# Kernel optimization log

Hardware: AMD Instinct MI355X
Metric: run time of the kernel (lower is better)

Reference implementation:

```python
import jax, jax.numpy as jnp
import numpy as np
import math

KERNEL_SIZES = [3, 5, 7, 7, 9, 9]
DILATIONS = [1, 2, 1, 3, 1, 2]
NUM_HEADS = 6
HEAD_DIM = 32  # in_channels 192 / 6 heads


def _neighborhood_patches(t, k, dil):
    """Equivalent of F.unfold(t, kernel_size=k, dilation=dil, padding=dil*(k//2)).
    t: [B, d, H, W] -> [B, d, k*k, H, W] (zero-padded borders, torch unfold ordering:
    patch index p = i*k + j over the kernel window, row-major)."""
    B, d, H, W = t.shape
    pad = dil * (k // 2)
    tp = jnp.pad(t, ((0, 0), (0, 0), (pad, pad), (pad, pad)))
    pats = [tp[:, :, i * dil:i * dil + H, j * dil:j * dil + W]
            for i in range(k) for j in range(k)]
    return jnp.stack(pats, axis=2)


def setup_inputs() -> dict:
    key = jax.random.key(0)
    ks = jax.random.split(key, 3 + NUM_HEADS)
    B, C, H, W = 4, 192, 96, 96
    x = jax.random.normal(ks[0], (B, C, H, W), dtype=jnp.float32)
    w_qkv = jax.random.normal(ks[1], (3 * C, C), dtype=jnp.float32) * 0.02  # 1x1 conv weight
    w_out = jax.random.normal(ks[2], (C, C), dtype=jnp.float32) * 0.02      # 1x1 conv weight
    inp = {"x": x, "w_qkv": w_qkv, "w_out": w_out}
    for i, k in enumerate(KERNEL_SIZES):
        # module inits biases to zeros; use small randn so softmax path is exercised
        inp[f"b{i}"] = jax.random.normal(ks[3 + i], (k * k,), dtype=jnp.float32) * 0.02
    return inp


def reference(x, w_qkv, w_out, b0, b1, b2, b3, b4, b5):
    biases = [b0, b1, b2, b3, b4, b5]
    B, C, H, W = x.shape
    scale = 1.0 / math.sqrt(HEAD_DIM)
    # 1x1 conv qkv projection
    qkv = jnp.einsum('bchw,oc->bohw', x, w_qkv)
    q, k, v = jnp.split(qkv, 3, axis=1)
    q = q.reshape(B, NUM_HEADS, HEAD_DIM, H, W)
    k = k.reshape(B, NUM_HEADS, HEAD_DIM, H, W)
    v = v.reshape(B, NUM_HEADS, HEAD_DIM, H, W)
    head_outs = []
    for i in range(NUM_HEADS):  # heads have structurally different (k, dilation)
        ksz, dil = KERNEL_SIZES[i], DILATIONS[i]
        kp = _neighborhood_patches(k[:, i], ksz, dil)  # [B, d, k*k, H, W]
        vp = _neighborhood_patches(v[:, i], ksz, dil)  # [B, d, k*k, H, W]
        scores = jnp.einsum('bdhw,bdphw->bphw', q[:, i], kp) * scale
        scores = scores + biases[i][None, :, None, None]
        attn = jax.nn.softmax(scores, axis=1)  # softmax over the k*k neighborhood
        head_outs.append(jnp.einsum('bphw,bdphw->bdhw', attn, vp))
    out = jnp.concatenate(head_outs, axis=1)  # [B, C, H, W]
    return jnp.einsum('bchw,oc->bohw', out, w_out)
```

## Files before the change

### kernel.cpp

```cpp
#include <hip/hip_runtime.h>
#include <hip/hip_bf16.h>
#include <math.h>

#define NPIX 9216
#define HDIM 96
#define WDIM 96
#define NHEADS 6
#define BATCH 4

typedef _Float16 f16x8 __attribute__((ext_vector_type(8)));
typedef float    f32x4 __attribute__((ext_vector_type(4)));

struct Bias6 { const float* p[6]; };

__device__ __forceinline__ void cp16(void* ldst, const void* gsrc) {
    __builtin_amdgcn_global_load_lds(
        (const __attribute__((address_space(1))) unsigned int*)gsrc,
        (__attribute__((address_space(3))) unsigned int*)ldst, 16, 0, 0);
}

__device__ __forceinline__ unsigned packf16(float a, float b) {
    _Float16 ha = (_Float16)a, hb = (_Float16)b;
    return (unsigned)*(unsigned short*)&ha | ((unsigned)*(unsigned short*)&hb << 16);
}

template<int N>
__device__ __forceinline__ void waitcnt_vm() {
    if constexpr (N == 0) asm volatile("s_waitcnt vmcnt(0)" ::: "memory");
    else if constexpr (N == 2) asm volatile("s_waitcnt vmcnt(2)" ::: "memory");
    else if constexpr (N == 3) asm volatile("s_waitcnt vmcnt(3)" ::: "memory");
    else if constexpr (N == 5) asm volatile("s_waitcnt vmcnt(5)" ::: "memory");
    else asm volatile("s_waitcnt vmcnt(0)" ::: "memory");
    __builtin_amdgcn_sched_barrier(0);
}

#define MIX_LL(acc, kk, qq) asm("v_fma_mix_f32 %0, %1, %2, %0 op_sel:[0,0,0] op_sel_hi:[1,1,0]" : "+v"(acc) : "v"(kk), "v"(qq))
#define MIX_HH(acc, kk, qq) asm("v_fma_mix_f32 %0, %1, %2, %0 op_sel:[1,1,0] op_sel_hi:[1,1,0]" : "+v"(acc) : "v"(kk), "v"(qq))
#define MIX_LF(acc, vv, ee) asm("v_fma_mix_f32 %0, %1, %2, %0 op_sel:[0,0,0] op_sel_hi:[1,0,0]" : "+v"(acc) : "v"(vv), "v"(ee))
#define MIX_HF(acc, vv, ee) asm("v_fma_mix_f32 %0, %1, %2, %0 op_sel:[1,0,0] op_sel_hi:[1,0,0]" : "+v"(acc) : "v"(vv), "v"(ee))

__global__ __launch_bounds__(256) void convert_x(
    const float* __restrict__ x, _Float16* __restrict__ Xf,
    const float* __restrict__ w1, _Float16* __restrict__ Wf1,
    const float* __restrict__ w2, _Float16* __restrict__ Wf2,
    uint4* __restrict__ guard)
{
    __shared__ float t[32][65];
    const int b  = blockIdx.z;
    const int c0 = blockIdx.y * 32;
    const int p0 = blockIdx.x * 64;
    const int tid = threadIdx.x;

    if (blockIdx.y == 0 && blockIdx.z == 0) {
        const int f = blockIdx.x * 256 + tid;
        #pragma unroll
        for (int u = 0; u < 4; ++u) {
            const int i = f * 4 + u;
            if (i < 576 * 192) Wf1[i] = (_Float16)w1[i];
            else               Wf2[i - 576 * 192] = (_Float16)w2[i - 576 * 192];
        }
        if (blockIdx.x == 0 && tid < 64)
            guard[tid] = make_uint4(0u, 0u, 0u, 0u);
    }

    const int pl = tid & 63;
    #pragma unroll
    for (int i = 0; i < 8; ++i) {
        const int c = i * 4 + (tid >> 6);
        t[c][pl] = x[((size_t)b * 192 + c0 + c) * NPIX + p0 + pl];
    }
    __syncthreads();
    const int p  = tid >> 2;
    const int cq = (tid & 3) * 8;
    f16x8 vh;
    #pragma unroll
    for (int j = 0; j < 8; ++j)
        vh[j] = (_Float16)t[cq + j][p];
    *(f16x8*)(Xf + ((size_t)b * NPIX + p0 + p) * 192 + c0 + cq) = vh;
}

template<int MODE, int M>
__global__ __launch_bounds__(256) void gemm_mfma(
    const _Float16* __restrict__ A, const _Float16* __restrict__ B,
    void* __restrict__ Yv)
{
    constexpr int MT = M / 64;
    __shared__ _Float16 sA[64 * 64];
    __shared__ _Float16 sB[128 * 64];

    const int orig = blockIdx.x;
    const int xcd = orig & 7;
    const int l = orig >> 3;
    const int m0 = (l % MT) * 64;
    const int b  = (l / MT) & 3;
    const int n0 = (xcd * 9 + l / (MT * 4)) * 128;

    const int tid  = threadIdx.x;
    const int lane = tid & 63;
    const int wid  = tid >> 6;
    const int wr = wid >> 1, wc = wid & 1;
    const int lr = lane & 15;
    const int kg = lane >> 4;

    const char* gA = (const char*)A + (size_t)m0 * 384;
    const char* gB = (const char*)B + ((size_t)b * NPIX + n0) * 384;

    f32x4 acc[2][4];
    #pragma unroll
    for (int mf = 0; mf < 2; ++mf)
        #pragma unroll
        for (int nf = 0; nf < 4; ++nf)
            acc[mf][nf] = (f32x4){0.f, 0.f, 0.f, 0.f};

    for (int ks = 0; ks < 3; ++ks) {
        if (ks) __syncthreads();
        const int kb = ks * 128;
        #pragma unroll
        for (int it = 0; it < 2; ++it) {
            const int d  = it * 256 + tid;
            const int rd = d >> 3, cd = d & 7;
            const size_t src = (size_t)rd * 384 + kb + ((cd ^ (rd & 7)) << 4);
            cp16((char*)sA + d * 16, gA + src);
        }
        #pragma unroll
        for (int it = 0; it < 4; ++it) {
            const int d  = it * 256 + tid;
            const int rd = d >> 3, cd = d & 7;
            const size_t src = (size_t)rd * 384 + kb + ((cd ^ (rd & 7)) << 4);
            cp16((char*)sB + d * 16, gB + src);
        }
        __syncthreads();
        #pragma unroll
        for (int s = 0; s < 2; ++s) {
            f16x8 aH[2], bH[4];
            #pragma unroll
            for (int mf = 0; mf < 2; ++mf) {
                const int row = wr * 32 + mf * 16 + lr;
                const int c = (s * 4 + kg) ^ (row & 7);
                aH[mf] = *(const f16x8*)((const char*)sA + row * 128 + c * 16);
            }
            #pragma unroll
            for (int nf = 0; nf < 4; ++nf) {
                const int row = wc * 64 + nf * 16 + lr;
                const int c = (s * 4 + kg) ^ (row & 7);
                bH[nf] = *(const f16x8*)((const char*)sB + row * 128 + c * 16);
            }
            #pragma unroll
            for (int mf = 0; mf < 2; ++mf)
                #pragma unroll
                for (int nf = 0; nf < 4; ++nf)
                    acc[mf][nf] = __builtin_amdgcn_mfma_f32_16x16x32_f16(aH[mf], bH[nf], acc[mf][nf], 0, 0, 0);
        }
    }

    if (MODE == 0) {
        float* Yb = (float*)Yv + ((size_t)b * M + m0 + wr * 32) * NPIX + n0 + wc * 64;
        #pragma unroll
        for (int mf = 0; mf < 2; ++mf)
            #pragma unroll
            for (int r = 0; r < 4; ++r) {
                const int row = mf * 16 + kg * 4 + r;
                #pragma unroll
                for (int nf = 0; nf < 4; ++nf)
                    Yb[(size_t)row * NPIX + nf * 16 + lr] = acc[mf][nf][r];
            }
    } else {
        #pragma unroll
        for (int mf = 0; mf < 2; ++mf) {
            const int cbase = m0 + wr * 32 + mf * 16 + kg * 4;
            unsigned* Yq = (unsigned*)Yv
                + (((size_t)b * 72 + (cbase >> 3)) * NPIX + n0 + wc * 64 + lr) * 4
                + ((kg & 1) << 1);
            #pragma unroll
            for (int nf = 0; nf < 4; ++nf) {
                Yq[(nf * 16) * 4 + 0] = packf16(acc[mf][nf][0], acc[mf][nf][1]);
                Yq[(nf * 16) * 4 + 1] = packf16(acc[mf][nf][2], acc[mf][nf][3]);
            }
        }
    }
}

template<int KSZ, int DIL, bool DB, int L>
__device__ __forceinline__ void attn_body(
    const uint4* __restrict__ Qq, const uint4* __restrict__ Kq,
    const uint4* __restrict__ Vq, const float* __restrict__ bias,
    const uint4* __restrict__ guard,
    _Float16* __restrict__ oh, int h0, int w0,
    uint4* __restrict__ bufs,
    unsigned (* __restrict__ out_lds)[256])
{
    constexpr int CC  = KSZ / 2;
    constexpr int HAL = CC * DIL;
    constexpr int R   = 8 + 2 * HAL;
    constexpr int C   = 32 + 2 * HAL;
    constexpr int RC  = R * C;
    constexpr int NN  = KSZ * KSZ;

    const int tid = threadIdx.x;
    const int tx = tid & 31;
    const int ty = tid >> 5;
    const int pix = (h0 + ty) * WDIM + (w0 + tx);
    const int lb = ty * C + tx;

    uint4 qv[4];
    #pragma unroll
    for (int p = 0; p < 4; ++p) qv[p] = Qq[(size_t)p * NPIX + pix];

    float score[NN];
    #pragma unroll
    for (int n = 0; n < NN; ++n) score[n] = bias[n] * 5.656854249492381f;

    auto STAGE = [&](int r) {
        const uint4* src = (r < 4) ? (Kq + (size_t)r * NPIX)
                                   : (Vq + (size_t)(r - 4) * NPIX);
        uint4* dst = bufs + (DB ? ((r & 1) * (L * 256)) : 0);
        #pragma unroll
        for (int it = 0; it < L; ++it) {
            const int idx = it * 256 + tid;
            const int rr = idx / C, cc = idx - rr * C;
            const int gh = h0 - HAL + rr, gw = w0 - HAL + cc;
            const bool ok = (idx < RC) && ((unsigned)gh < (unsigned)HDIM)
                                       && ((unsigned)gw < (unsigned)WDIM);
            const uint4* s = ok ? (src + gh * WDIM + gw) : guard;
            cp16(dst + idx, s);
        }
    };

    auto QK = [&](const uint4* buf, int oct) {
        const uint4 q = qv[oct];
        #pragma unroll
        for (int i = 0; i < KSZ; ++i)
            #pragma unroll
            for (int j = 0; j < KSZ; ++j) {
                const uint4 k8 = buf[lb + i * DIL * C + j * DIL];
                float s = score[i * KSZ + j];
                MIX_LL(s, k8.x, q.x); MIX_HH(s, k8.x, q.x);
                MIX_LL(s, k8.y, q.y); MIX_HH(s, k8.y, q.y);
                MIX_LL(s, k8.z, q.z); MIX_HH(s, k8.z, q.z);
                MIX_LL(s, k8.w, q.w); MIX_HH(s, k8.w, q.w);
                score[i * KSZ + j] = s;
            }
    };

    float inv = 0.f;
    auto SOFTMAX = [&]() {
        float l = 0.f;
        #pragma unroll
        for (int n = 0; n < NN; ++n) {
            const float e = exp2f(score[n] * 0.25506113952980654f);
            l += e;
            score[n] = e;
        }
        inv = 1.f / l;
    };

    auto PV = [&](const uint4* buf, int oct) {
        float a0 = 0.f, a1 = 0.f, a2 = 0.f, a3 = 0.f;
        float a4 = 0.f, a5 = 0.f, a6 = 0.f, a7 = 0.f;
        #pragma unroll
        for (int i = 0; i < KSZ; ++i)
            #pragma unroll
            for (int j = 0; j < KSZ; ++j) {
                const uint4 v8 = buf[lb + i * DIL * C + j * DIL];
                const float e = score[i * KSZ + j];
                MIX_LF(a0, v8.x, e); MIX_HF(a1, v8.x, e);
                MIX_LF(a2, v8.y, e); MIX_HF(a3, v8.y, e);
                MIX_LF(a4, v8.z, e); MIX_HF(a5, v8.z, e);
                MIX_LF(a6, v8.w, e); MIX_HF(a7, v8.w, e);
            }
        const int rr = oct & 1;
        out_lds[rr * 4 + 0][tid] = packf16(a0 * inv, a1 * inv);
        out_lds[rr * 4 + 1][tid] = packf16(a2 * inv, a3 * inv);
        out_lds[rr * 4 + 2][tid] = packf16(a4 * inv, a5 * inv);
        out_lds[rr * 4 + 3][tid] = packf16(a6 * inv, a7 * inv);
    };

    auto COOP = [&](int half) {
        #pragma unroll
        for (int it = 0; it < 2; ++it) {
            const int linear = it * 256 + tid;
            const int px = linear >> 1;
            const int c  = linear & 1;
            const int gpix = (h0 + (px >> 5)) * WDIM + w0 + (px & 31);
            uint4 val = make_uint4(out_lds[c * 4 + 0][px], out_lds[c * 4 + 1][px],
                                   out_lds[c * 4 + 2][px], out_lds[c * 4 + 3][px]);
            *((uint4*)((unsigned*)(oh + (size_t)gpix * 192)) + half * 2 + c) = val;
        }
    };

    if constexpr (DB) {
        STAGE(0);
        #pragma unroll
        for (int r = 0; r < 8; ++r) {
            if (r < 7) STAGE(r + 1);
            if (r < 7) waitcnt_vm<L>(); else waitcnt_vm<0>();
            __builtin_amdgcn_s_barrier();
            __builtin_amdgcn_sched_barrier(0);
            const uint4* buf = bufs + (r & 1) * (L * 256);
            if (r < 4) {
                QK(buf, r);
                if (r == 3) SOFTMAX();
            } else {
                PV(buf, r - 4);
                asm volatile("s_waitcnt lgkmcnt(0)" ::: "memory");
                __builtin_amdgcn_sched_barrier(0);
            }
            __builtin_amdgcn_s_barrier();
            __builtin_amdgcn_sched_barrier(0);
            if (r == 5) COOP(0);
            if (r == 7) COOP(1);
        }
    } else {
        #pragma unroll
        for (int r = 0; r < 8; ++r) {
            __syncthreads();
            if (r == 6) COOP(0);
            STAGE(r);
            __syncthreads();
            const uint4* buf = bufs;
            if (r < 4) {
                QK(buf, r);
                if (r == 3) SOFTMAX();
            } else {
                PV(buf, r - 4);
            }
        }
        __syncthreads();
        COOP(1);
    }
}

__global__ __launch_bounds__(256) void attn_kernel(
    const uint4* __restrict__ qkv, Bias6 bs, _Float16* __restrict__ ATf,
    const uint4* __restrict__ guard)
{
    __shared__ uint4 bufs[1536];
    __shared__ unsigned out_lds[8][256];

    const int orig = blockIdx.x;
    const int wg = (orig & 7) * 108 + (orig >> 3);
    const int panel = wg / 36;
    const int tile = wg - panel * 36;
    const int chunk = panel / 3, slot = panel - chunk * 3;
    int head, b;
    if (slot == 0)      { head = 4 + (chunk >> 2); b = chunk & 3; }
    else if (slot == 1) { head = 2 + (chunk >> 2); b = chunk & 3; }
    else                { head = (chunk < 4) ? 1 : 0; b = chunk & 3; }
    const int tx = tile % 3, ty = tile / 3;
    const int w0 = tx * 32, h0 = ty * 8;

    const uint4* base = qkv + (size_t)b * 72 * NPIX;
    const uint4* Qq = base + (size_t)(head * 4) * NPIX;
    const uint4* Kq = base + (size_t)(24 + head * 4) * NPIX;
    const uint4* Vq = base + (size_t)(48 + head * 4) * NPIX;
    _Float16* oh = ATf + (size_t)b * NPIX * 192 + head * 32;
    const float* bias = bs.p[head];

    switch (head) {
        case 0: attn_body<3, 1, true, 2>(Qq, Kq, Vq, bias, guard, oh, h0, w0, bufs, out_lds); break;
        case 1: attn_body<5, 2, true, 3>(Qq, Kq, Vq, bias, guard, oh, h0, w0, bufs, out_lds); break;
        case 2: attn_body<7, 1, true, 3>(Qq, Kq, Vq, bias, guard, oh, h0, w0, bufs, out_lds); break;
        case 3: attn_body<7, 3, false, 6>(Qq, Kq, Vq, bias, guard, oh, h0, w0, bufs, out_lds); break;
        case 4: attn_body<9, 1, true, 3>(Qq, Kq, Vq, bias, guard, oh, h0, w0, bufs, out_lds); break;
        case 5: attn_body<9, 2, false, 5>(Qq, Kq, Vq, bias, guard, oh, h0, w0, bufs, out_lds); break;
    }
}

extern "C" void kernel_launch(void* const* d_in, const int* in_sizes, int n_in,
                              void* d_out, int out_size, void* d_ws, size_t ws_size,
                              hipStream_t stream) {
    const float* x     = (const float*)d_in[0];
    const float* w_qkv = (const float*)d_in[1];
    const float* w_out = (const float*)d_in[2];
    Bias6 bs;
    for (int i = 0; i < 6; ++i) bs.p[i] = (const float*)d_in[3 + i];
    float* out = (float*)d_out;

    char* ws = (char*)d_ws;
    uint4*    QKV = (uint4*)ws;         ws += (size_t)BATCH * 72 * NPIX * 16;
    _Float16* Xf  = (_Float16*)ws;      ws += (size_t)BATCH * NPIX * 192 * 2;
    _Float16* ATf = (_Float16*)ws;      ws += (size_t)BATCH * NPIX * 192 * 2;
    _Float16* Wf1 = (_Float16*)ws;      ws += (size_t)576 * 192 * 2;
    _Float16* Wf2 = (_Float16*)ws;      ws += (size_t)192 * 192 * 2;
    uint4* guard  = (uint4*)ws;         ws += 1024;

    convert_x<<<dim3(NPIX / 64, 192 / 32, BATCH), 256, 0, stream>>>(
        x, Xf, w_qkv, Wf1, w_out, Wf2, guard);

    gemm_mfma<1, 576><<<dim3(8 * (576 / 64) * 4 * 9), 256, 0, stream>>>(
        Wf1, Xf, (void*)QKV);

    attn_kernel<<<dim3(864), 256, 0, stream>>>(QKV, bs, ATf, guard);

    gemm_mfma<0, 192><<<dim3(8 * (192 / 64) * 4 * 9), 256, 0, stream>>>(
        Wf2, ATf, (void*)out);
}
```

Before: 83.89 us.

## Triple-buffer K/V staging to drop the per-step trailing barrier

The double-buffered attention path now rotates through three LDS staging buffers, so each step needs only one barrier instead of two. The LDS wait is merged into the global-load wait. The output staging area is doubled so each PV octet writes its own rows, and the first half of the output store moves to step 6. This targets barrier stalls between the K/V stages, at the cost of much more LDS per block, which may lower the number of blocks resident per CU.

```diff
diff --git a/kernel.cpp b/kernel.cpp
--- a/kernel.cpp
+++ b/kernel.cpp
@@ -25,12 +25,11 @@
 }
 
 template<int N>
-__device__ __forceinline__ void waitcnt_vm() {
-    if constexpr (N == 0) asm volatile("s_waitcnt vmcnt(0)" ::: "memory");
-    else if constexpr (N == 2) asm volatile("s_waitcnt vmcnt(2)" ::: "memory");
-    else if constexpr (N == 3) asm volatile("s_waitcnt vmcnt(3)" ::: "memory");
-    else if constexpr (N == 5) asm volatile("s_waitcnt vmcnt(5)" ::: "memory");
-    else asm volatile("s_waitcnt vmcnt(0)" ::: "memory");
+__device__ __forceinline__ void wait_vm_lgkm() {
+    if constexpr (N == 0) asm volatile("s_waitcnt vmcnt(0) lgkmcnt(0)" ::: "memory");
+    else if constexpr (N == 2) asm volatile("s_waitcnt vmcnt(2) lgkmcnt(0)" ::: "memory");
+    else if constexpr (N == 3) asm volatile("s_waitcnt vmcnt(3) lgkmcnt(0)" ::: "memory");
+    else asm volatile("s_waitcnt vmcnt(0) lgkmcnt(0)" ::: "memory");
     __builtin_amdgcn_sched_barrier(0);
 }
 
@@ -180,6 +179,9 @@
     }
 }
 
+#define TW 32
+#define TH 8
+
 template<int KSZ, int DIL, bool DB, int L>
 __device__ __forceinline__ void attn_body(
     const uint4* __restrict__ Qq, const uint4* __restrict__ Kq,
@@ -191,8 +193,8 @@
 {
     constexpr int CC  = KSZ / 2;
     constexpr int HAL = CC * DIL;
-    constexpr int R   = 8 + 2 * HAL;
-    constexpr int C   = 32 + 2 * HAL;
+    constexpr int R   = TH + 2 * HAL;
+    constexpr int C   = TW + 2 * HAL;
     constexpr int RC  = R * C;
     constexpr int NN  = KSZ * KSZ;
 
@@ -213,7 +215,7 @@
     auto STAGE = [&](int r) {
         const uint4* src = (r < 4) ? (Kq + (size_t)r * NPIX)
                                    : (Vq + (size_t)(r - 4) * NPIX);
-        uint4* dst = bufs + (DB ? ((r & 1) * (L * 256)) : 0);
+        uint4* dst = bufs + (DB ? ((r % 3) * (L * 256)) : 0);
         #pragma unroll
         for (int it = 0; it < L; ++it) {
             const int idx = it * 256 + tid;
@@ -268,11 +270,10 @@
                 MIX_LF(a4, v8.z, e); MIX_HF(a5, v8.z, e);
                 MIX_LF(a6, v8.w, e); MIX_HF(a7, v8.w, e);
             }
-        const int rr = oct & 1;
-        out_lds[rr * 4 + 0][tid] = packf16(a0 * inv, a1 * inv);
-        out_lds[rr * 4 + 1][tid] = packf16(a2 * inv, a3 * inv);
-        out_lds[rr * 4 + 2][tid] = packf16(a4 * inv, a5 * inv);
-        out_lds[rr * 4 + 3][tid] = packf16(a6 * inv, a7 * inv);
+        out_lds[oct * 4 + 0][tid] = packf16(a0 * inv, a1 * inv);
+        out_lds[oct * 4 + 1][tid] = packf16(a2 * inv, a3 * inv);
+        out_lds[oct * 4 + 2][tid] = packf16(a4 * inv, a5 * inv);
+        out_lds[oct * 4 + 3][tid] = packf16(a6 * inv, a7 * inv);
     };
 
     auto COOP = [&](int half) {
@@ -282,8 +283,10 @@
             const int px = linear >> 1;
             const int c  = linear & 1;
             const int gpix = (h0 + (px >> 5)) * WDIM + w0 + (px & 31);
-            uint4 val = make_uint4(out_lds[c * 4 + 0][px], out_lds[c * 4 + 1][px],
-                                   out_lds[c * 4 + 2][px], out_lds[c * 4 + 3][px]);
+            uint4 val = make_uint4(out_lds[half * 8 + c * 4 + 0][px],
+                                   out_lds[half * 8 + c * 4 + 1][px],
+                                   out_lds[half * 8 + c * 4 + 2][px],
+                                   out_lds[half * 8 + c * 4 + 3][px]);
             *((uint4*)((unsigned*)(oh + (size_t)gpix * 192)) + half * 2 + c) = val;
         }
     };
@@ -293,23 +296,23 @@
         #pragma unroll
         for (int r = 0; r < 8; ++r) {
             if (r < 7) STAGE(r + 1);
-            if (r < 7) waitcnt_vm<L>(); else waitcnt_vm<0>();
+            if (r < 7) wait_vm_lgkm<L>(); else wait_vm_lgkm<0>();
             __builtin_amdgcn_s_barrier();
             __builtin_amdgcn_sched_barrier(0);
-            const uint4* buf = bufs + (r & 1) * (L * 256);
+            if (r == 6) COOP(0);
+            const uint4* buf = bufs + (r % 3) * (L * 256);
             if (r < 4) {
                 QK(buf, r);
                 if (r == 3) SOFTMAX();
             } else {
                 PV(buf, r - 4);
-                asm volatile("s_waitcnt lgkmcnt(0)" ::: "memory");
-                __builtin_amdgcn_sched_barrier(0);
-            }
-            __builtin_amdgcn_s_barrier();
-            __builtin_amdgcn_sched_barrier(0);
-            if (r == 5) COOP(0);
-            if (r == 7) COOP(1);
-        }
+            }
+        }
+        asm volatile("s_waitcnt lgkmcnt(0)" ::: "memory");
+        __builtin_amdgcn_sched_barrier(0);
+        __builtin_amdgcn_s_barrier();
+        __builtin_amdgcn_sched_barrier(0);
+        COOP(1);
     } else {
         #pragma unroll
         for (int r = 0; r < 8; ++r) {
@@ -334,8 +337,8 @@
     const uint4* __restrict__ qkv, Bias6 bs, _Float16* __restrict__ ATf,
     const uint4* __restrict__ guard)
 {
-    __shared__ uint4 bufs[1536];
-    __shared__ unsigned out_lds[8][256];
+    __shared__ uint4 bufs[2304];
+    __shared__ unsigned out_lds[16][256];
 
     const int orig = blockIdx.x;
     const int wg = (orig & 7) * 108 + (orig >> 3);
@@ -346,8 +349,8 @@
     if (slot == 0)      { head = 4 + (chunk >> 2); b = chunk & 3; }
     else if (slot == 1) { head = 2 + (chunk >> 2); b = chunk & 3; }
     else                { head = (chunk < 4) ? 1 : 0; b = chunk & 3; }
-    const int tx = tile % 3, ty = tile / 3;
-    const int w0 = tx * 32, h0 = ty * 8;
+    const int txt = tile % 3, tyt = tile / 3;
+    const int w0 = txt * TW, h0 = tyt * TH;
 
     const uint4* base = qkv + (size_t)b * 72 * NPIX;
     const uint4* Qq = base + (size_t)(head * 4) * NPIX;
```

Measured after the change: 85.35 us. About the same (+1.7%).
